# Performance work log

Hardware: AMD Instinct MI355X
Metric: run time of the kernel (lower is better)

The kernel has to match this reference:

```python
import jax, jax.numpy as jnp
import numpy as np

B, N, L, E = 8, 2000, 128, 2048  # batch, nodes, local_size+1, ff_hidden_dim
PENALTY = 10.0


def setup_inputs() -> dict:
    key = jax.random.key(0)
    ks = jax.random.split(key, 8)
    dist = jax.random.uniform(ks[0], (B, N, N), jnp.float32) + 1e-3  # positive distances
    theta = jax.random.normal(ks[1], (B, N, N), jnp.float32)
    ins_feature0 = jax.random.normal(ks[2], (B, N, 1), jnp.float32)
    ins_feature1 = jax.random.normal(ks[3], (B, N, 1), jnp.float32)
    d_in = 2 * L + 2
    W1 = jax.random.normal(ks[4], (d_in, E), jnp.float32) * 0.02
    b1 = jnp.zeros((E,), jnp.float32)
    W2 = jax.random.normal(ks[5], (E, L), jnp.float32) * 0.02
    b2 = jnp.zeros((L,), jnp.float32)
    return {"theta": theta, "dist": dist, "ins_feature0": ins_feature0,
            "ins_feature1": ins_feature1, "W1": W1, "b1": b1, "W2": W2, "b2": b2}


def reference(theta, dist, ins_feature0, ins_feature1, W1, b1, W2, b2):
    k = W2.shape[1]  # local_size (L)
    # smallest-k along last dim, sorted ascending (torch.topk largest=False)
    neg_vals, idx = jax.lax.top_k(-dist, k)          # [B,N,L]
    sorted_dist = -neg_vals
    sorted_dist = sorted_dist / jnp.max(sorted_dist, axis=-1, keepdims=True)
    sorted_theta = jnp.take_along_axis(theta, idx, axis=-1)  # [B,N,L]
    x_in = jnp.concatenate([sorted_dist, sorted_theta, ins_feature0, ins_feature1], axis=-1)  # [B,N,2L+2]
    edge_emb = x_in @ W1 + b1                        # [B,N,E] (no nonlinearity, as in source)
    out = edge_emb @ W2 + b2 - sorted_dist           # [B,N,L]
    b_, n_, _ = dist.shape
    bi = jnp.arange(b_)[:, None, None]
    ni = jnp.arange(n_)[None, :, None]
    out_mat = jnp.full(dist.shape, PENALTY, dist.dtype).at[bi, ni, idx].set(out)
    return out_mat
```

## Files before the change

### kernel.cpp

```cpp
#include <hip/hip_runtime.h>
#include <hip/hip_bf16.h>

#define BN 8
#define NN 2000
#define LL 128
#define EE 2048
#define DIN 258
#define KPAD 264
#define NROWS (BN*NN)
#define PENALTY_V 10.0f
#define NBINS 1024
#define CANDCAP 256
#define SPLITK 16
#define ECHUNK (EE/SPLITK)

__global__ __launch_bounds__(256) void kA1(const float* __restrict__ W1,
                                           const float* __restrict__ b1,
                                           const float* __restrict__ W2,
                                           float* __restrict__ part) {
    __shared__ float As2[8][64];
    const int t = threadIdx.x;
    const int j = t & 127;
    const int half = t >> 7;
    const int rg = blockIdx.x >> 4;
    const int ks = blockIdx.x & 15;
    const int k0 = rg * 8;
    const int ebase = ks * ECHUNK;
    float acc[4] = {0.f, 0.f, 0.f, 0.f};
    for (int ec = ebase; ec < ebase + ECHUNK; ec += 64) {
        #pragma unroll
        for (int q = 0; q < 2; ++q) {
            int linear = q * 256 + t;
            int r8 = linear >> 6;
            int e  = linear & 63;
            int k  = k0 + r8;
            float v;
            if (k < DIN)       v = W1[k * EE + ec + e];
            else if (k == DIN) v = b1[ec + e];
            else               v = 0.0f;
            As2[r8][e] = v;
        }
        __syncthreads();
        #pragma unroll 8
        for (int e = 0; e < 64; ++e) {
            float w = W2[(ec + e) * LL + j];
            #pragma unroll
            for (int rr = 0; rr < 4; ++rr)
                acc[rr] += As2[half * 4 + rr][e] * w;
        }
        __syncthreads();
    }
    #pragma unroll
    for (int rr = 0; rr < 4; ++rr) {
        int k = k0 + half * 4 + rr;
        part[(size_t)ks * (KPAD * LL) + k * LL + j] = acc[rr];
    }
}

__global__ __launch_bounds__(256) void kA2(const float* __restrict__ part,
                                           const float* __restrict__ b2,
                                           float* __restrict__ Wc,
                                           float* __restrict__ bc) {
    const int i = blockIdx.x * 256 + threadIdx.x;
    float s = 0.f;
    #pragma unroll
    for (int q = 0; q < SPLITK; ++q) s += part[(size_t)q * (KPAD * LL) + i];
    const int k = i >> 7;
    const int j = i & 127;
    if (k == DIN)      { bc[j] = s + b2[j]; Wc[i] = 0.f; }
    else if (k > DIN)  { Wc[i] = 0.f; }
    else               { Wc[i] = s; }
}

__global__ __launch_bounds__(256) void kB(const float* __restrict__ dist,
                                          const float* __restrict__ theta,
                                          const float* __restrict__ f0,
                                          const float* __restrict__ f1,
                                          float* __restrict__ xin,
                                          int*   __restrict__ gidx) {
    __shared__ unsigned int hist[NBINS];
    __shared__ unsigned int starts[NBINS];
    __shared__ unsigned long long cand[CANDCAP];
    __shared__ unsigned int wred[4];
    __shared__ float s_od[LL];
    __shared__ int   s_oi[LL];
    __shared__ float s_oth[LL];

    const int t = threadIdx.x;
    const int lane = t & 63;
    const int w = t >> 6;
    const int row = blockIdx.x;

    #pragma unroll
    for (int q = 0; q < NBINS / 256; ++q) hist[t + q * 256] = 0u;
    cand[t & (CANDCAP - 1)] = ~0ULL;

    unsigned int v[8];
    const bool has = (t < 250);
    unsigned int lmax = 0u;
    if (has) {
        const uint4* drow4 = (const uint4*)(dist + (size_t)row * NN);
        uint4 a = drow4[2 * t];
        uint4 b = drow4[2 * t + 1];
        v[0] = a.x; v[1] = a.y; v[2] = a.z; v[3] = a.w;
        v[4] = b.x; v[5] = b.y; v[6] = b.z; v[7] = b.w;
        #pragma unroll
        for (int k = 0; k < 8; ++k) lmax = max(lmax, v[k]);
    }
    #pragma unroll
    for (int d = 32; d > 0; d >>= 1) lmax = max(lmax, (unsigned int)__shfl_down((int)lmax, d));
    if (lane == 0) wred[w] = lmax;
    __syncthreads();

    const unsigned int vmax_bits = max(max(wred[0], wred[1]), max(wred[2], wred[3]));
    const float scale = (float)(NBINS - 1) / __uint_as_float(vmax_bits);

    int bk[8];
    if (has) {
        #pragma unroll
        for (int k = 0; k < 8; ++k) {
            float f = __uint_as_float(v[k]);
            int b = (int)(f * scale);
            bk[k] = b < 0 ? 0 : (b > NBINS - 1 ? NBINS - 1 : b);
            atomicAdd(&hist[bk[k]], 1u);
        }
    }
    __syncthreads();

    {
        const int base = t * (NBINS / 256);
        unsigned int loc[NBINS / 256];
        unsigned int run = 0;
        #pragma unroll
        for (int q = 0; q < NBINS / 256; ++q) { loc[q] = run; run += hist[base + q]; }
        unsigned int inc = run;
        #pragma unroll
        for (int d = 1; d < 64; d <<= 1) {
            unsigned int o = (unsigned int)__shfl_up((int)inc, d);
            if (lane >= d) inc += o;
        }
        if (lane == 63) wred[w] = inc;
        __syncthreads();
        unsigned int woff = 0;
        for (int k = 0; k < 4; ++k) if (k < w) woff += wred[k];
        const unsigned int texcl = woff + inc - run;
        #pragma unroll
        for (int q = 0; q < NBINS / 256; ++q) {
            unsigned int e = texcl + loc[q];
            hist[base + q] = e;
            starts[base + q] = e;
        }
    }
    __syncthreads();

    if (has) {
        #pragma unroll
        for (int k = 0; k < 8; ++k) {
            if (starts[bk[k]] < (unsigned int)LL) {
                unsigned int pos = atomicAdd(&hist[bk[k]], 1u);
                if (pos < CANDCAP)
                    cand[pos] = ((unsigned long long)v[k] << 32) | (unsigned int)(8 * t + k);
            }
        }
    }
    __syncthreads();

    {
        const unsigned long long key = cand[t];
        if (key != ~0ULL) {
            const unsigned int bits = (unsigned int)(key >> 32);
            const unsigned int idx  = (unsigned int)key;
            const float th = theta[(size_t)row * NN + idx];
            float f = __uint_as_float(bits);
            int b = (int)(f * scale);
            b = b < 0 ? 0 : (b > NBINS - 1 ? NBINS - 1 : b);
            unsigned int s = starts[b];
            unsigned int e = hist[b];
            if (e > CANDCAP) e = CANDCAP;
            unsigned int r = s;
            for (unsigned int j = s; j < e; ++j) r += (cand[j] < key);
            if (r < (unsigned int)LL) {
                s_od[r]  = f;
                s_oi[r]  = (int)idx;
                s_oth[r] = th;
            }
        }
    }
    __syncthreads();

    const float dmax = s_od[LL - 1];
    float* xrow = xin + (size_t)row * KPAD;
    if (t < LL) {
        gidx[(size_t)row * LL + t] = s_oi[t];
        xrow[t] = s_od[t] / dmax;
        xrow[LL + t] = s_oth[t];
    } else if (t == LL) {
        xrow[256] = f0[row];
        xrow[257] = f1[row];
        #pragma unroll
        for (int z = DIN; z < KPAD; ++z) xrow[z] = 0.0f;
    }
}

__global__ __launch_bounds__(256) void kC(const float* __restrict__ xin,
                                          const float* __restrict__ Wc,
                                          const float* __restrict__ bc,
                                          float* __restrict__ val) {
    __shared__ __align__(16) float As[8][132];
    __shared__ __align__(16) float Bs[8][128];
    const int t = threadIdx.x;
    const int tr = t >> 4, tc = t & 15;
    const int row0 = blockIdx.x * 128;
    float acc[8][8];
    #pragma unroll
    for (int i = 0; i < 8; ++i)
        #pragma unroll
        for (int j = 0; j < 8; ++j) acc[i][j] = 0.f;

    for (int kc = 0; kc < KPAD; kc += 8) {
        #pragma unroll
        for (int q = 0; q < 4; ++q) {
            int linear = q * 256 + t;
            int m = linear >> 3, k = linear & 7;
            As[k][m] = xin[(size_t)(row0 + m) * KPAD + kc + k];
        }
        #pragma unroll
        for (int q = 0; q < 4; ++q) {
            int linear = q * 256 + t;
            int k = linear >> 7, c = linear & 127;
            Bs[k][c] = Wc[(kc + k) * LL + c];
        }
        __syncthreads();
        #pragma unroll
        for (int k = 0; k < 8; ++k) {
            float a[8], b[8];
            *(float4*)&a[0] = *(const float4*)&As[k][tr * 8];
            *(float4*)&a[4] = *(const float4*)&As[k][tr * 8 + 4];
            *(float4*)&b[0] = *(const float4*)&Bs[k][tc * 8];
            *(float4*)&b[4] = *(const float4*)&Bs[k][tc * 8 + 4];
            #pragma unroll
            for (int i = 0; i < 8; ++i)
                #pragma unroll
                for (int j = 0; j < 8; ++j)
                    acc[i][j] += a[i] * b[j];
        }
        __syncthreads();
    }
    #pragma unroll
    for (int i = 0; i < 8; ++i) {
        int r = row0 + tr * 8 + i;
        #pragma unroll
        for (int j = 0; j < 8; ++j) {
            int c = tc * 8 + j;
            val[(size_t)r * LL + c] = acc[i][j] + bc[c] - xin[(size_t)r * KPAD + c];
        }
    }
}

__global__ __launch_bounds__(256) void kD(const int* __restrict__ gidx,
                                          const float* __restrict__ val,
                                          float* __restrict__ out) {
    __shared__ __align__(16) float rowbuf[NN];
    const int t = threadIdx.x;
    const int row = blockIdx.x;
    for (int i = t; i < NN; i += 256) rowbuf[i] = PENALTY_V;
    __syncthreads();
    if (t < 128) rowbuf[gidx[(size_t)row * LL + t]] = val[(size_t)row * LL + t];
    __syncthreads();
    float4* out4 = (float4*)(out + (size_t)row * NN);
    const float4* rb4 = (const float4*)rowbuf;
    for (int q = t; q < NN / 4; q += 256) out4[q] = rb4[q];
}

extern "C" void kernel_launch(void* const* d_in, const int* in_sizes, int n_in,
                              void* d_out, int out_size, void* d_ws, size_t ws_size,
                              hipStream_t stream) {
    const float* theta = (const float*)d_in[0];
    const float* dist  = (const float*)d_in[1];
    const float* f0    = (const float*)d_in[2];
    const float* f1    = (const float*)d_in[3];
    const float* W1    = (const float*)d_in[4];
    const float* b1    = (const float*)d_in[5];
    const float* W2    = (const float*)d_in[6];
    const float* b2    = (const float*)d_in[7];
    float* out = (float*)d_out;

    char* ws = (char*)d_ws;
    float* Wc   = (float*)ws;
    float* bc   = (float*)(ws + 135168);
    float* xin  = (float*)(ws + 135680);
    int*   gidx = (int*)  (ws + 135680 + 16896000);
    float* val  = (float*)(ws + 135680 + 16896000 + 8192000);
    float* part = val;

    kA1<<<33 * SPLITK, 256, 0, stream>>>(W1, b1, W2, part);
    kA2<<<(KPAD * LL) / 256, 256, 0, stream>>>(part, b2, Wc, bc);
    kB<<<NROWS, 256, 0, stream>>>(dist, theta, f0, f1, xin, gidx);
    kC<<<NROWS / 128, 256, 0, stream>>>(xin, Wc, bc, val);
    kD<<<NROWS, 256, 0, stream>>>(gidx, val, out);
}
```

Measured before the change: 142.4 us.

## Run top-k selection one wavefront per row without block barriers

Measured after the change: 145.3 us. 2.1% more time.

```diff
diff --git a/kernel.cpp b/kernel.cpp
--- a/kernel.cpp
+++ b/kernel.cpp
@@ -9,10 +9,11 @@
 #define KPAD 264
 #define NROWS (BN*NN)
 #define PENALTY_V 10.0f
-#define NBINS 1024
+#define NBINS 512
 #define CANDCAP 256
 #define SPLITK 16
 #define ECHUNK (EE/SPLITK)
+#define RPB 4
 
 __global__ __launch_bounds__(256) void kA1(const float* __restrict__ W1,
                                            const float* __restrict__ b1,
@@ -78,127 +79,143 @@
                                           const float* __restrict__ f1,
                                           float* __restrict__ xin,
                                           int*   __restrict__ gidx) {
-    __shared__ unsigned int hist[NBINS];
-    __shared__ unsigned int starts[NBINS];
-    __shared__ unsigned long long cand[CANDCAP];
-    __shared__ unsigned int wred[4];
-    __shared__ float s_od[LL];
-    __shared__ int   s_oi[LL];
-    __shared__ float s_oth[LL];
+    __shared__ __align__(16) unsigned int hist_all[RPB][NBINS];
+    __shared__ __align__(16) unsigned long long cand_all[RPB][CANDCAP];
+    __shared__ __align__(16) float obuf_all[RPB][2 * LL];
+    __shared__ __align__(16) int   oidx_all[RPB][LL];
+    __shared__ float sdm[RPB];
 
     const int t = threadIdx.x;
     const int lane = t & 63;
     const int w = t >> 6;
-    const int row = blockIdx.x;
-
-    #pragma unroll
-    for (int q = 0; q < NBINS / 256; ++q) hist[t + q * 256] = 0u;
-    cand[t & (CANDCAP - 1)] = ~0ULL;
-
-    unsigned int v[8];
-    const bool has = (t < 250);
+    const int row = blockIdx.x * RPB + w;
+
+    unsigned int* hist = hist_all[w];
+    unsigned long long* cand = cand_all[w];
+    float* obuf = obuf_all[w];
+    int* oidx = oidx_all[w];
+
+    {
+        uint4 z4 = {0u, 0u, 0u, 0u};
+        #pragma unroll
+        for (int q = 0; q < NBINS / 256; ++q)
+            *(uint4*)&hist[(lane + q * 64) * 4] = z4;
+        unsigned long long f1v = ~0ULL;
+        #pragma unroll
+        for (int q = 0; q < CANDCAP / 64; ++q)
+            cand[lane + q * 64] = f1v;
+    }
+
+    unsigned int v[32];
+    const int nv = (lane < 52) ? 32 : 28;
+    {
+        const uint4* drow4 = (const uint4*)(dist + (size_t)row * NN);
+        #pragma unroll
+        for (int q = 0; q < 8; ++q) {
+            int qi = q * 64 + lane;
+            if (qi < NN / 4) {
+                uint4 a = drow4[qi];
+                v[4 * q]     = a.x;
+                v[4 * q + 1] = a.y;
+                v[4 * q + 2] = a.z;
+                v[4 * q + 3] = a.w;
+            }
+        }
+    }
+
     unsigned int lmax = 0u;
-    if (has) {
-        const uint4* drow4 = (const uint4*)(dist + (size_t)row * NN);
-        uint4 a = drow4[2 * t];
-        uint4 b = drow4[2 * t + 1];
-        v[0] = a.x; v[1] = a.y; v[2] = a.z; v[3] = a.w;
-        v[4] = b.x; v[5] = b.y; v[6] = b.z; v[7] = b.w;
-        #pragma unroll
-        for (int k = 0; k < 8; ++k) lmax = max(lmax, v[k]);
-    }
-    #pragma unroll
-    for (int d = 32; d > 0; d >>= 1) lmax = max(lmax, (unsigned int)__shfl_down((int)lmax, d));
-    if (lane == 0) wred[w] = lmax;
-    __syncthreads();
-
-    const unsigned int vmax_bits = max(max(wred[0], wred[1]), max(wred[2], wred[3]));
-    const float scale = (float)(NBINS - 1) / __uint_as_float(vmax_bits);
-
-    int bk[8];
-    if (has) {
-        #pragma unroll
-        for (int k = 0; k < 8; ++k) {
+    #pragma unroll
+    for (int k = 0; k < 32; ++k) if (k < nv) lmax = max(lmax, v[k]);
+    #pragma unroll
+    for (int d = 1; d < 64; d <<= 1) lmax = max(lmax, (unsigned int)__shfl_xor((int)lmax, d));
+    const float scale = (float)(NBINS - 1) / __uint_as_float(lmax);
+
+    #pragma unroll
+    for (int k = 0; k < 32; ++k) {
+        if (k < nv) {
             float f = __uint_as_float(v[k]);
             int b = (int)(f * scale);
-            bk[k] = b < 0 ? 0 : (b > NBINS - 1 ? NBINS - 1 : b);
-            atomicAdd(&hist[bk[k]], 1u);
-        }
-    }
-    __syncthreads();
+            b = b > NBINS - 1 ? NBINS - 1 : b;
+            atomicAdd(&hist[b], 1u);
+        }
+    }
 
     {
-        const int base = t * (NBINS / 256);
-        unsigned int loc[NBINS / 256];
-        unsigned int run = 0;
-        #pragma unroll
-        for (int q = 0; q < NBINS / 256; ++q) { loc[q] = run; run += hist[base + q]; }
+        uint4* h4 = (uint4*)&hist[lane * 8];
+        uint4 a0 = h4[0], a1 = h4[1];
+        unsigned int c[8] = {a0.x, a0.y, a0.z, a0.w, a1.x, a1.y, a1.z, a1.w};
+        unsigned int loc[8], run = 0;
+        #pragma unroll
+        for (int k = 0; k < 8; ++k) { loc[k] = run; run += c[k]; }
         unsigned int inc = run;
         #pragma unroll
         for (int d = 1; d < 64; d <<= 1) {
             unsigned int o = (unsigned int)__shfl_up((int)inc, d);
             if (lane >= d) inc += o;
         }
-        if (lane == 63) wred[w] = inc;
-        __syncthreads();
-        unsigned int woff = 0;
-        for (int k = 0; k < 4; ++k) if (k < w) woff += wred[k];
-        const unsigned int texcl = woff + inc - run;
-        #pragma unroll
-        for (int q = 0; q < NBINS / 256; ++q) {
-            unsigned int e = texcl + loc[q];
-            hist[base + q] = e;
-            starts[base + q] = e;
-        }
-    }
-    __syncthreads();
-
-    if (has) {
-        #pragma unroll
-        for (int k = 0; k < 8; ++k) {
-            if (starts[bk[k]] < (unsigned int)LL) {
-                unsigned int pos = atomicAdd(&hist[bk[k]], 1u);
-                if (pos < CANDCAP)
-                    cand[pos] = ((unsigned long long)v[k] << 32) | (unsigned int)(8 * t + k);
-            }
-        }
-    }
-    __syncthreads();
-
-    {
-        const unsigned long long key = cand[t];
-        if (key != ~0ULL) {
-            const unsigned int bits = (unsigned int)(key >> 32);
-            const unsigned int idx  = (unsigned int)key;
-            const float th = theta[(size_t)row * NN + idx];
+        const unsigned int excl = inc - run;
+        uint4 s0 = {excl + loc[0], excl + loc[1], excl + loc[2], excl + loc[3]};
+        uint4 s1 = {excl + loc[4], excl + loc[5], excl + loc[6], excl + loc[7]};
+        h4[0] = s0; h4[1] = s1;
+    }
+
+    #pragma unroll
+    for (int k = 0; k < 32; ++k) {
+        if (k < nv) {
+            unsigned int bits = v[k];
             float f = __uint_as_float(bits);
             int b = (int)(f * scale);
-            b = b < 0 ? 0 : (b > NBINS - 1 ? NBINS - 1 : b);
-            unsigned int s = starts[b];
-            unsigned int e = hist[b];
-            if (e > CANDCAP) e = CANDCAP;
-            unsigned int r = s;
-            for (unsigned int j = s; j < e; ++j) r += (cand[j] < key);
+            b = b > NBINS - 1 ? NBINS - 1 : b;
+            unsigned int old = atomicAdd(&hist[b], 0x10000u);
+            unsigned int start = old & 0xFFFFu;
+            if (start < (unsigned int)LL) {
+                unsigned int slot = start + (old >> 16);
+                unsigned int idx = (unsigned int)((k >> 2) * 256 + lane * 4 + (k & 3));
+                if (slot < (unsigned int)CANDCAP)
+                    cand[slot] = ((unsigned long long)bits << 32) | idx;
+            }
+        }
+    }
+
+    #pragma unroll
+    for (int s = 0; s < CANDCAP / 64; ++s) {
+        unsigned long long key = cand[lane + s * 64];
+        if (key != ~0ULL) {
+            unsigned int bits = (unsigned int)(key >> 32);
+            unsigned int idx  = (unsigned int)key;
+            float th = theta[(size_t)row * NN + idx];
+            float f = __uint_as_float(bits);
+            int b = (int)(f * scale);
+            b = b > NBINS - 1 ? NBINS - 1 : b;
+            unsigned int word = hist[b];
+            unsigned int start = word & 0xFFFFu;
+            unsigned int end = start + (word >> 16);
+            if (end > (unsigned int)CANDCAP) end = (unsigned int)CANDCAP;
+            unsigned int r = start;
+            for (unsigned int j = start; j < end; ++j) r += (cand[j] < key);
             if (r < (unsigned int)LL) {
-                s_od[r]  = f;
-                s_oi[r]  = (int)idx;
-                s_oth[r] = th;
+                obuf[r] = f;
+                obuf[LL + r] = th;
+                oidx[r] = (int)idx;
+                if (r == LL - 1) sdm[w] = f;
             }
         }
     }
-    __syncthreads();
-
-    const float dmax = s_od[LL - 1];
-    float* xrow = xin + (size_t)row * KPAD;
-    if (t < LL) {
-        gidx[(size_t)row * LL + t] = s_oi[t];
-        xrow[t] = s_od[t] / dmax;
-        xrow[LL + t] = s_oth[t];
-    } else if (t == LL) {
-        xrow[256] = f0[row];
-        xrow[257] = f1[row];
-        #pragma unroll
-        for (int z = DIN; z < KPAD; ++z) xrow[z] = 0.0f;
+
+    {
+        const float rdm = 1.0f / sdm[w];
+        float* xrow = xin + (size_t)row * KPAD;
+        float4 o = *(float4*)&obuf[lane * 4];
+        if (lane < 32) { o.x *= rdm; o.y *= rdm; o.z *= rdm; o.w *= rdm; }
+        *(float4*)&xrow[lane * 4] = o;
+        if (lane == 0) {
+            xrow[256] = f0[row];
+            xrow[257] = f1[row];
+            #pragma unroll
+            for (int z = DIN; z < KPAD; ++z) xrow[z] = 0.0f;
+        }
+        int2 g = *(int2*)&oidx[lane * 2];
+        *(int2*)&gidx[(size_t)row * LL + lane * 2] = g;
     }
 }
 
@@ -295,7 +312,7 @@
 
     kA1<<<33 * SPLITK, 256, 0, stream>>>(W1, b1, W2, part);
     kA2<<<(KPAD * LL) / 256, 256, 0, stream>>>(part, b2, Wc, bc);
-    kB<<<NROWS, 256, 0, stream>>>(dist, theta, f0, f1, xin, gidx);
+    kB<<<NROWS / RPB, 256, 0, stream>>>(dist, theta, f0, f1, xin, gidx);
     kC<<<NROWS / 128, 256, 0, stream>>>(xin, Wc, bc, val);
     kD<<<NROWS, 256, 0, stream>>>(gidx, val, out);
 }
```
